# Kernel tuning notes

Measured on AMD Instinct MI355X. Metric: run time of the kernel, lower is better.

## Reference

```python
import jax, jax.numpy as jnp
import numpy as np

D_MODEL = 512
HEADS = 8
WIN = 16
LN_EPS = 1e-5


def setup_inputs() -> dict:
    key = jax.random.key(0)
    ks = jax.random.split(key, 5)
    B, T = 2, 4096
    s = 1.0 / np.sqrt(D_MODEL)
    x = jax.random.normal(ks[0], (B, T, D_MODEL), dtype=jnp.float32)
    Wq = jax.random.normal(ks[1], (D_MODEL, D_MODEL), dtype=jnp.float32) * s
    Wk = jax.random.normal(ks[2], (D_MODEL, D_MODEL), dtype=jnp.float32) * s
    Wv = jax.random.normal(ks[3], (D_MODEL, D_MODEL), dtype=jnp.float32) * s
    Wp = jax.random.normal(ks[4], (D_MODEL, D_MODEL), dtype=jnp.float32) * s
    ln_gamma = jnp.ones((D_MODEL,), dtype=jnp.float32)
    ln_beta = jnp.zeros((D_MODEL,), dtype=jnp.float32)
    return {"x": x, "Wq": Wq, "Wk": Wk, "Wv": Wv, "Wp": Wp,
            "ln_gamma": ln_gamma, "ln_beta": ln_beta}


def _local_attention(x, Wq, Wk, Wv, Wp, ln_gamma, ln_beta):
    B, T, D = x.shape
    H = HEADS
    d = D // H
    scale = d ** (-0.5)
    # projections (torch Linear: y = x @ W^T)
    q = (x @ Wq.T).reshape(B, T, H, d)
    k = (x @ Wk.T).reshape(B, T, H, d)
    v = (x @ Wv.T).reshape(B, T, H, d)
    offs = jnp.arange(-WIN, WIN + 1)                      # [W]
    pos = jnp.arange(T)[:, None] + offs[None, :]          # [T, W]
    valid = (pos >= 0) & (pos < T)                        # [T, W]
    idx = jnp.clip(pos, 0, T - 1)                         # [T, W]
    k_win = k[:, idx]                                     # [B, T, W, H, d]
    v_win = v[:, idx]                                     # [B, T, W, H, d]
    scores = jnp.einsum('bthd,btwhd->bthw', q, k_win) * scale
    scores = jnp.where(valid[None, :, None, :], scores, -jnp.inf)
    attn = jax.nn.softmax(scores, axis=-1)                # over window
    out = jnp.einsum('bthw,btwhd->bthd', attn, v_win).reshape(B, T, D)
    y = x + out @ Wp.T                                    # residual + proj
    mu = jnp.mean(y, axis=-1, keepdims=True)
    var = jnp.mean(jnp.square(y - mu), axis=-1, keepdims=True)
    return ln_gamma * (y - mu) * jax.lax.rsqrt(var + LN_EPS) + ln_beta


def reference(x, Wq, Wk, Wv, Wp, ln_gamma, ln_beta):
    return _local_attention(x, Wq, Wk, Wv, Wp, ln_gamma, ln_beta)
```

## Files before the change

### kernel.cpp

```cpp
#include <hip/hip_runtime.h>
#include <hip/hip_bf16.h>
#include <stdint.h>

typedef __bf16 bf16;
typedef __attribute__((ext_vector_type(8))) __bf16 bf16x8;
typedef __attribute__((ext_vector_type(2))) __bf16 bf16x2;
typedef __attribute__((ext_vector_type(4))) float f32x4;
typedef __attribute__((ext_vector_type(4))) unsigned int u32x4;

#define GLOAD16(gsrc, ldst)                                              \
  __builtin_amdgcn_global_load_lds(                                      \
      (const __attribute__((address_space(1))) unsigned int*)(gsrc),     \
      (__attribute__((address_space(3))) unsigned int*)(ldst), 16, 0, 0)

static constexpr int T_LEN = 4096;
static constexpr int WIN = 16;

__device__ __forceinline__ bf16x8 cvt8(float4 a, float4 b) {
  bf16x8 o;
  o[0] = (bf16)a.x; o[1] = (bf16)a.y; o[2] = (bf16)a.z; o[3] = (bf16)a.w;
  o[4] = (bf16)b.x; o[5] = (bf16)b.y; o[6] = (bf16)b.z; o[7] = (bf16)b.w;
  return o;
}

__global__ __launch_bounds__(256) void prep_kernel(const float* __restrict__ x,
                                                   const float* __restrict__ wq,
                                                   const float* __restrict__ wk,
                                                   const float* __restrict__ wv,
                                                   const float* __restrict__ wp,
                                                   bf16* __restrict__ xb,
                                                   bf16* __restrict__ wqkv,
                                                   bf16* __restrict__ wpb) {
  int bid = blockIdx.x;
  if (bid < 2048) {
    int i = bid * 256 + threadIdx.x;
    const float4* s4 = (const float4*)x + (size_t)i * 2;
    ((bf16x8*)xb)[i] = cvt8(s4[0], s4[1]);
  } else {
    int i = (bid - 2048) * 256 + threadIdx.x;
    int which = i >> 15;
    int j = i & 32767;
    const float* src = (which == 0) ? wq : (which == 1) ? wk : (which == 2) ? wv : wp;
    bf16* dst = (which < 3) ? (wqkv + (size_t)which * 512 * 512) : wpb;
    const float4* s4 = (const float4*)src + (size_t)j * 2;
    ((bf16x8*)dst)[j] = cvt8(s4[0], s4[1]);
  }
}

__global__ __launch_bounds__(256) void gemm_qkv_kernel(const bf16* __restrict__ Ab,
                                                       const bf16* __restrict__ Bw,
                                                       bf16* __restrict__ Cb) {
  constexpr int K = 512, BK = 64, NIT = K / BK;
  __shared__ __align__(16) bf16 SMEM[16384];
  const int tid = threadIdx.x;
  const int l = tid & 63;
  const int w = tid >> 6;
  const int g = l >> 4;
  const int c = l & 15;
  int bid = blockIdx.x;
  bid = (bid & 7) * 96 + (bid >> 3);
  const int m0 = (bid / 12) * 128;
  const int n0 = (bid % 12) * 128;

  const f32x4 zero = {0.f, 0.f, 0.f, 0.f};
  f32x4 acc[4][4];
#pragma unroll
  for (int i = 0; i < 4; ++i)
#pragma unroll
    for (int j = 0; j < 4; ++j) acc[i][j] = zero;

  const int wm = (w >> 1) * 64;
  const int wn = (w & 1) * 64;
  const int cx = c & 7;

#pragma unroll 1
  for (int t = 0; t < NIT; ++t) {
    const int k0 = t * BK;
#pragma unroll
    for (int i = 0; i < 4; ++i) {
      int s = tid + i * 256;
      int row = s >> 3;
      int j = s & 7;
      int ksrc = k0 + ((j ^ (row & 7)) << 3);
      GLOAD16(Ab + (size_t)(m0 + row) * 512 + ksrc, &SMEM[s * 8]);
      GLOAD16(Bw + (size_t)(n0 + row) * 512 + ksrc, &SMEM[8192 + s * 8]);
    }
    __syncthreads();
#pragma unroll
    for (int kk = 0; kk < 2; ++kk) {
      const int joff = ((kk * 4 + g) ^ cx) << 3;
      bf16x8 af[4], bfr[4];
#pragma unroll
      for (int mi = 0; mi < 4; ++mi)
        af[mi] = *(const bf16x8*)&SMEM[(wm + mi * 16 + c) * 64 + joff];
#pragma unroll
      for (int ni = 0; ni < 4; ++ni)
        bfr[ni] = *(const bf16x8*)&SMEM[8192 + (wn + ni * 16 + c) * 64 + joff];
#pragma unroll
      for (int mi = 0; mi < 4; ++mi)
#pragma unroll
        for (int ni = 0; ni < 4; ++ni)
          acc[mi][ni] = __builtin_amdgcn_mfma_f32_16x16x32_bf16(af[mi], bfr[ni], acc[mi][ni], 0, 0, 0);
    }
    __syncthreads();
  }

  bf16* Cw = &SMEM[w * 4096];
  const int r0 = (l >> 4) * 4;
#pragma unroll
  for (int mi = 0; mi < 4; ++mi)
#pragma unroll
    for (int ni = 0; ni < 4; ++ni)
#pragma unroll
      for (int r = 0; r < 4; ++r)
        Cw[(mi * 16 + r0 + r) * 64 + ni * 16 + c] = (bf16)acc[mi][ni][r];
#pragma unroll
  for (int i = 0; i < 8; ++i) {
    int row = (l >> 3) + 8 * i;
    bf16x8 v = *(const bf16x8*)&Cw[row * 64 + (l & 7) * 8];
    *(bf16x8*)(Cb + (size_t)(m0 + wm + row) * 1536 + n0 + wn + (l & 7) * 8) = v;
  }
}

static constexpr int TCB = 64;
static constexpr int NP = 96;
static constexpr int KST = 72;
static constexpr int NPT = 112;

__global__ __launch_bounds__(256) void attn_kernel(const bf16* __restrict__ qkv,
                                                   bf16* __restrict__ aout) {
  __shared__ __align__(16) bf16 Kl[NP * KST];
  __shared__ __align__(16) unsigned short Vt[64 * NPT];
  __shared__ __align__(16) bf16 QPO[4 * 16 * 72];

  const int tid = threadIdx.x;
  const int wid = tid >> 6;
  const int l = tid & 63;
  const int g = l >> 4;
  const int c = l & 15;

  const int bid = blockIdx.x;
  const int chunk = bid & 63;
  const int h = (bid >> 6) & 7;
  const int b = bid >> 9;
  const int t0 = chunk * TCB;
  const int base = b * T_LEN;

#pragma unroll
  for (int i = 0; i < 3; ++i) {
    int task = tid + i * 256;
    int p = task >> 3;
    int c8 = (task & 7) * 8;
    int pg = min(max(t0 - WIN + p, 0), T_LEN - 1);
    const bf16* kr = qkv + (size_t)(base + pg) * 1536 + 512 + h * 64 + c8;
    const bf16* vr = qkv + (size_t)(base + pg) * 1536 + 1024 + h * 64 + c8;
    *(bf16x8*)&Kl[p * KST + c8] = *(const bf16x8*)kr;
    bf16x8 vv = *(const bf16x8*)vr;
#pragma unroll
    for (int e = 0; e < 8; ++e)
      Vt[(c8 + e) * NPT + p] = ((const unsigned short*)&vv)[e];
  }
#pragma unroll
  for (int i = 0; i < 2; ++i) {
    int task = tid + i * 256;
    int p = task >> 3;
    int c8 = (task & 7) * 8;
    const bf16* qr = qkv + (size_t)(base + t0 + p) * 1536 + h * 64 + c8;
    *(bf16x8*)&QPO[(p >> 4) * 1152 + (p & 15) * 72 + c8] = *(const bf16x8*)qr;
  }
  {
    int d = tid >> 2;
    int p0 = 96 + (tid & 3) * 4;
    *(uint2*)&Vt[d * NPT + p0] = make_uint2(0u, 0u);
  }
  __syncthreads();

  const int tg = t0 + wid * 16;
  const float scale = 0.125f;

  bf16* Qw = &QPO[wid * 1152];
  bf16x8 qf0 = *(const bf16x8*)&Qw[c * 72 + g * 8];
  bf16x8 qf1 = *(const bf16x8*)&Qw[c * 72 + 32 + g * 8];

  const f32x4 zero = {0.f, 0.f, 0.f, 0.f};
  const u32x4 zu = {0u, 0u, 0u, 0u};

  f32x4 st[3];
#pragma unroll
  for (int wt = 0; wt < 3; ++wt) {
    int rk = 16 * wid + 16 * wt + c;
    bf16x8 ka0 = *(const bf16x8*)&Kl[rk * KST + g * 8];
    bf16x8 ka1 = *(const bf16x8*)&Kl[rk * KST + 32 + g * 8];
    f32x4 t = __builtin_amdgcn_mfma_f32_16x16x32_bf16(ka0, qf0, zero, 0, 0, 0);
    st[wt] = __builtin_amdgcn_mfma_f32_16x16x32_bf16(ka1, qf1, t, 0, 0, 0);
  }

  float pv[3][4];
  float lsum = 0.f;
#pragma unroll
  for (int wt = 0; wt < 3; ++wt)
#pragma unroll
    for (int r = 0; r < 4; ++r) {
      int w = 16 * wt + 4 * g + r;
      int pos = tg - WIN + w;
      bool valid = (w >= c) && (w <= c + 32) && (pos >= 0) && (pos < T_LEN);
      float e = __expf(st[wt][r] * scale);
      pv[wt][r] = valid ? e : 0.f;
      lsum += pv[wt][r];
    }
  lsum += __shfl_xor(lsum, 16);
  lsum += __shfl_xor(lsum, 32);
  float inv = 1.f / lsum;

  bf16* P = Qw;
#pragma unroll
  for (int wt = 0; wt < 3; ++wt) {
    bf16x2 p01, p23;
    p01[0] = (bf16)(pv[wt][0] * inv);
    p01[1] = (bf16)(pv[wt][1] * inv);
    p23[0] = (bf16)(pv[wt][2] * inv);
    p23[1] = (bf16)(pv[wt][3] * inv);
    *(bf16x2*)&P[c * 56 + 16 * wt + 4 * g]     = p01;
    *(bf16x2*)&P[c * 56 + 16 * wt + 4 * g + 2] = p23;
  }

  bf16x8 pa0 = *(const bf16x8*)&P[c * 56 + 8 * g];
  int g1 = (g < 2) ? g : 1;
  bf16x8 pa1 = *(const bf16x8*)&P[c * 56 + 32 + 8 * g1];
  if (g >= 2) pa1 = __builtin_bit_cast(bf16x8, zu);

  f32x4 acc[4] = {zero, zero, zero, zero};
#pragma unroll
  for (int dt = 0; dt < 4; ++dt) {
    const unsigned short* vp = &Vt[(16 * dt + c) * NPT + 16 * wid + 8 * g];
    bf16x8 v0 = *(const bf16x8*)(vp);
    bf16x8 v1 = *(const bf16x8*)(vp + 32);
    acc[dt] = __builtin_amdgcn_mfma_f32_16x16x32_bf16(pa0, v0, acc[dt], 0, 0, 0);
    acc[dt] = __builtin_amdgcn_mfma_f32_16x16x32_bf16(pa1, v1, acc[dt], 0, 0, 0);
  }

  bf16* O = Qw;
#pragma unroll
  for (int dt = 0; dt < 4; ++dt)
#pragma unroll
    for (int r = 0; r < 4; ++r)
      O[(4 * g + r) * 72 + 16 * dt + c] = (bf16)acc[dt][r];

  bf16x8 o0 = *(const bf16x8*)&O[c * 72 + g * 8];
  bf16x8 o1 = *(const bf16x8*)&O[c * 72 + 32 + g * 8];
  bf16* orow = aout + (size_t)(base + tg + c) * 512 + h * 64;
  *(bf16x8*)(orow + g * 8) = o0;
  *(bf16x8*)(orow + 32 + g * 8) = o1;
}

__global__ __launch_bounds__(512) void proj_ln_kernel(const bf16* __restrict__ A,
                                                      const bf16* __restrict__ Bw,
                                                      const float* __restrict__ X,
                                                      const float* __restrict__ gamma,
                                                      const float* __restrict__ beta,
                                                      float* __restrict__ out) {
  constexpr int K = 512, BK = 64, BM = 32, NIT = K / BK;
  __shared__ __align__(16) bf16 As[BM * BK];
  __shared__ __align__(16) bf16 Bs[512 * BK];
  __shared__ __align__(16) float rsum[32][8];
  __shared__ __align__(16) float rsq[32][8];

  const int tid = threadIdx.x;
  const int w = tid >> 6;
  const int l = tid & 63;
  const int g = l >> 4;
  const int c = l & 15;
  const int cx = c & 7;
  int bid = blockIdx.x;
  bid = (bid & 7) * 32 + (bid >> 3);
  const int m0 = bid * BM;

  const f32x4 zero = {0.f, 0.f, 0.f, 0.f};
  f32x4 acc[2][4];
#pragma unroll
  for (int m = 0; m < 2; ++m)
#pragma unroll
    for (int n = 0; n < 4; ++n) acc[m][n] = zero;

#pragma unroll 1
  for (int t = 0; t < NIT; ++t) {
    const int k0 = t * BK;
    if (tid < 256) {
      int row = tid >> 3;
      int j = tid & 7;
      GLOAD16(A + (size_t)(m0 + row) * 512 + k0 + ((j ^ (row & 7)) << 3), &As[tid * 8]);
    }
#pragma unroll
    for (int i = 0; i < 8; ++i) {
      int s = tid + i * 512;
      int row = s >> 3;
      int j = s & 7;
      GLOAD16(Bw + (size_t)row * 512 + k0 + ((j ^ (row & 7)) << 3), &Bs[s * 8]);
    }
    __syncthreads();
#pragma unroll
    for (int kk = 0; kk < 2; ++kk) {
      const int joff = ((kk * 4 + g) ^ cx) << 3;
      bf16x8 af[2], bfv[4];
#pragma unroll
      for (int m = 0; m < 2; ++m)
        af[m] = *(const bf16x8*)&As[(m * 16 + c) * 64 + joff];
#pragma unroll
      for (int n = 0; n < 4; ++n)
        bfv[n] = *(const bf16x8*)&Bs[(w * 64 + n * 16 + c) * 64 + joff];
#pragma unroll
      for (int m = 0; m < 2; ++m)
#pragma unroll
        for (int n = 0; n < 4; ++n)
          acc[m][n] = __builtin_amdgcn_mfma_f32_16x16x32_bf16(af[m], bfv[n], acc[m][n], 0, 0, 0);
    }
    __syncthreads();
  }

  const int col0 = w * 64 + c;
  float ps[2][4], ps2[2][4];
#pragma unroll
  for (int m = 0; m < 2; ++m)
#pragma unroll
    for (int r = 0; r < 4; ++r) {
      int row = m0 + m * 16 + 4 * g + r;
      float s = 0.f, s2 = 0.f;
#pragma unroll
      for (int n = 0; n < 4; ++n) {
        float y = acc[m][n][r] + X[(size_t)row * 512 + col0 + n * 16];
        acc[m][n][r] = y;
        s += y;
        s2 += y * y;
      }
      ps[m][r] = s;
      ps2[m][r] = s2;
    }
#pragma unroll
  for (int m = 0; m < 2; ++m)
#pragma unroll
    for (int r = 0; r < 4; ++r) {
      float s = ps[m][r], s2 = ps2[m][r];
      s += __shfl_xor(s, 1);  s2 += __shfl_xor(s2, 1);
      s += __shfl_xor(s, 2);  s2 += __shfl_xor(s2, 2);
      s += __shfl_xor(s, 4);  s2 += __shfl_xor(s2, 4);
      s += __shfl_xor(s, 8);  s2 += __shfl_xor(s2, 8);
      ps[m][r] = s;
      ps2[m][r] = s2;
    }
  if (c == 0) {
#pragma unroll
    for (int m = 0; m < 2; ++m)
#pragma unroll
      for (int r = 0; r < 4; ++r) {
        rsum[m * 16 + 4 * g + r][w] = ps[m][r];
        rsq[m * 16 + 4 * g + r][w] = ps2[m][r];
      }
  }
  __syncthreads();

  float gam[4], bet[4];
#pragma unroll
  for (int n = 0; n < 4; ++n) {
    gam[n] = gamma[col0 + n * 16];
    bet[n] = beta[col0 + n * 16];
  }
#pragma unroll
  for (int m = 0; m < 2; ++m)
#pragma unroll
    for (int r = 0; r < 4; ++r) {
      int rl = m * 16 + 4 * g + r;
      float4 s0 = *(const float4*)&rsum[rl][0];
      float4 s1 = *(const float4*)&rsum[rl][4];
      float4 q0 = *(const float4*)&rsq[rl][0];
      float4 q1 = *(const float4*)&rsq[rl][4];
      float sum = (s0.x + s0.y + s0.z + s0.w) + (s1.x + s1.y + s1.z + s1.w);
      float sq  = (q0.x + q0.y + q0.z + q0.w) + (q1.x + q1.y + q1.z + q1.w);
      float mu = sum * (1.f / 512.f);
      float var = sq * (1.f / 512.f) - mu * mu;
      float rs = rsqrtf(var + 1e-5f);
#pragma unroll
      for (int n = 0; n < 4; ++n)
        out[(size_t)(m0 + rl) * 512 + col0 + n * 16] =
            gam[n] * (acc[m][n][r] - mu) * rs + bet[n];
    }
}

extern "C" void kernel_launch(void* const* d_in, const int* in_sizes, int n_in,
                              void* d_out, int out_size, void* d_ws, size_t ws_size,
                              hipStream_t stream) {
  const float* x  = (const float*)d_in[0];
  const float* Wq = (const float*)d_in[1];
  const float* Wk = (const float*)d_in[2];
  const float* Wv = (const float*)d_in[3];
  const float* Wp = (const float*)d_in[4];
  const float* g  = (const float*)d_in[5];
  const float* be = (const float*)d_in[6];
  float* out = (float*)d_out;

  char* ws = (char*)d_ws;
  bf16* xb   = (bf16*)(ws);
  bf16* wqkv = (bf16*)(ws + 8388608);
  bf16* wpb  = (bf16*)(ws + 9961472);
  bf16* qkv  = (bf16*)(ws + 10485760);
  bf16* aout = (bf16*)(ws + 35651584);

  prep_kernel<<<2560, 256, 0, stream>>>(x, Wq, Wk, Wv, Wp, xb, wqkv, wpb);
  gemm_qkv_kernel<<<64 * 12, 256, 0, stream>>>(xb, wqkv, qkv);
  attn_kernel<<<1024, 256, 0, stream>>>(qkv, aout);
  proj_ln_kernel<<<256, 512, 0, stream>>>(aout, wpb, x, g, be, out);
}
```

Measured before the change: 60.81 us.

## Fuse sliding-window attention into projection+LayerNorm kernel, keep attention output in LDS

Merges the attention kernel into the output-projection/LayerNorm kernel. Each 512-thread block computes attention for its 32 rows across all 8 heads in two passes of 4 heads, writes the result into an LDS tile, then runs the Wp GEMM directly from that tile. This removes one kernel launch and the global write and read of the intermediate attention output. In exchange, only 256 blocks do the attention work (previously 1024), LDS use per block is large (~127KB), and the K/V windows are loaded per 32-row block with more halo overlap.

Result: faster. 59.58 us (-2.0%).

```diff
diff --git a/kernel.cpp b/kernel.cpp
--- a/kernel.cpp
+++ b/kernel.cpp
@@ -62,16 +62,16 @@
   const int m0 = (bid / 12) * 128;
   const int n0 = (bid % 12) * 128;
 
-  const f32x4 zero = {0.f, 0.f, 0.f, 0.f};
-  f32x4 acc[4][4];
-#pragma unroll
-  for (int i = 0; i < 4; ++i)
-#pragma unroll
-    for (int j = 0; j < 4; ++j) acc[i][j] = zero;
-
   const int wm = (w >> 1) * 64;
   const int wn = (w & 1) * 64;
   const int cx = c & 7;
+
+  const f32x4 zero = {0.f, 0.f, 0.f, 0.f};
+  f32x4 acc[4][4];
+#pragma unroll
+  for (int i = 0; i < 4; ++i)
+#pragma unroll
+    for (int j = 0; j < 4; ++j) acc[i][j] = zero;
 
 #pragma unroll 1
   for (int t = 0; t < NIT; ++t) {
@@ -122,148 +122,16 @@
   }
 }
 
-static constexpr int TCB = 64;
-static constexpr int NP = 96;
-static constexpr int KST = 72;
-static constexpr int NPT = 112;
-
-__global__ __launch_bounds__(256) void attn_kernel(const bf16* __restrict__ qkv,
-                                                   bf16* __restrict__ aout) {
-  __shared__ __align__(16) bf16 Kl[NP * KST];
-  __shared__ __align__(16) unsigned short Vt[64 * NPT];
-  __shared__ __align__(16) bf16 QPO[4 * 16 * 72];
-
-  const int tid = threadIdx.x;
-  const int wid = tid >> 6;
-  const int l = tid & 63;
-  const int g = l >> 4;
-  const int c = l & 15;
-
-  const int bid = blockIdx.x;
-  const int chunk = bid & 63;
-  const int h = (bid >> 6) & 7;
-  const int b = bid >> 9;
-  const int t0 = chunk * TCB;
-  const int base = b * T_LEN;
-
-#pragma unroll
-  for (int i = 0; i < 3; ++i) {
-    int task = tid + i * 256;
-    int p = task >> 3;
-    int c8 = (task & 7) * 8;
-    int pg = min(max(t0 - WIN + p, 0), T_LEN - 1);
-    const bf16* kr = qkv + (size_t)(base + pg) * 1536 + 512 + h * 64 + c8;
-    const bf16* vr = qkv + (size_t)(base + pg) * 1536 + 1024 + h * 64 + c8;
-    *(bf16x8*)&Kl[p * KST + c8] = *(const bf16x8*)kr;
-    bf16x8 vv = *(const bf16x8*)vr;
-#pragma unroll
-    for (int e = 0; e < 8; ++e)
-      Vt[(c8 + e) * NPT + p] = ((const unsigned short*)&vv)[e];
-  }
-#pragma unroll
-  for (int i = 0; i < 2; ++i) {
-    int task = tid + i * 256;
-    int p = task >> 3;
-    int c8 = (task & 7) * 8;
-    const bf16* qr = qkv + (size_t)(base + t0 + p) * 1536 + h * 64 + c8;
-    *(bf16x8*)&QPO[(p >> 4) * 1152 + (p & 15) * 72 + c8] = *(const bf16x8*)qr;
-  }
-  {
-    int d = tid >> 2;
-    int p0 = 96 + (tid & 3) * 4;
-    *(uint2*)&Vt[d * NPT + p0] = make_uint2(0u, 0u);
-  }
-  __syncthreads();
-
-  const int tg = t0 + wid * 16;
-  const float scale = 0.125f;
-
-  bf16* Qw = &QPO[wid * 1152];
-  bf16x8 qf0 = *(const bf16x8*)&Qw[c * 72 + g * 8];
-  bf16x8 qf1 = *(const bf16x8*)&Qw[c * 72 + 32 + g * 8];
-
-  const f32x4 zero = {0.f, 0.f, 0.f, 0.f};
-  const u32x4 zu = {0u, 0u, 0u, 0u};
-
-  f32x4 st[3];
-#pragma unroll
-  for (int wt = 0; wt < 3; ++wt) {
-    int rk = 16 * wid + 16 * wt + c;
-    bf16x8 ka0 = *(const bf16x8*)&Kl[rk * KST + g * 8];
-    bf16x8 ka1 = *(const bf16x8*)&Kl[rk * KST + 32 + g * 8];
-    f32x4 t = __builtin_amdgcn_mfma_f32_16x16x32_bf16(ka0, qf0, zero, 0, 0, 0);
-    st[wt] = __builtin_amdgcn_mfma_f32_16x16x32_bf16(ka1, qf1, t, 0, 0, 0);
-  }
-
-  float pv[3][4];
-  float lsum = 0.f;
-#pragma unroll
-  for (int wt = 0; wt < 3; ++wt)
-#pragma unroll
-    for (int r = 0; r < 4; ++r) {
-      int w = 16 * wt + 4 * g + r;
-      int pos = tg - WIN + w;
-      bool valid = (w >= c) && (w <= c + 32) && (pos >= 0) && (pos < T_LEN);
-      float e = __expf(st[wt][r] * scale);
-      pv[wt][r] = valid ? e : 0.f;
-      lsum += pv[wt][r];
-    }
-  lsum += __shfl_xor(lsum, 16);
-  lsum += __shfl_xor(lsum, 32);
-  float inv = 1.f / lsum;
-
-  bf16* P = Qw;
-#pragma unroll
-  for (int wt = 0; wt < 3; ++wt) {
-    bf16x2 p01, p23;
-    p01[0] = (bf16)(pv[wt][0] * inv);
-    p01[1] = (bf16)(pv[wt][1] * inv);
-    p23[0] = (bf16)(pv[wt][2] * inv);
-    p23[1] = (bf16)(pv[wt][3] * inv);
-    *(bf16x2*)&P[c * 56 + 16 * wt + 4 * g]     = p01;
-    *(bf16x2*)&P[c * 56 + 16 * wt + 4 * g + 2] = p23;
-  }
-
-  bf16x8 pa0 = *(const bf16x8*)&P[c * 56 + 8 * g];
-  int g1 = (g < 2) ? g : 1;
-  bf16x8 pa1 = *(const bf16x8*)&P[c * 56 + 32 + 8 * g1];
-  if (g >= 2) pa1 = __builtin_bit_cast(bf16x8, zu);
-
-  f32x4 acc[4] = {zero, zero, zero, zero};
-#pragma unroll
-  for (int dt = 0; dt < 4; ++dt) {
-    const unsigned short* vp = &Vt[(16 * dt + c) * NPT + 16 * wid + 8 * g];
-    bf16x8 v0 = *(const bf16x8*)(vp);
-    bf16x8 v1 = *(const bf16x8*)(vp + 32);
-    acc[dt] = __builtin_amdgcn_mfma_f32_16x16x32_bf16(pa0, v0, acc[dt], 0, 0, 0);
-    acc[dt] = __builtin_amdgcn_mfma_f32_16x16x32_bf16(pa1, v1, acc[dt], 0, 0, 0);
-  }
-
-  bf16* O = Qw;
-#pragma unroll
-  for (int dt = 0; dt < 4; ++dt)
-#pragma unroll
-    for (int r = 0; r < 4; ++r)
-      O[(4 * g + r) * 72 + 16 * dt + c] = (bf16)acc[dt][r];
-
-  bf16x8 o0 = *(const bf16x8*)&O[c * 72 + g * 8];
-  bf16x8 o1 = *(const bf16x8*)&O[c * 72 + 32 + g * 8];
-  bf16* orow = aout + (size_t)(base + tg + c) * 512 + h * 64;
-  *(bf16x8*)(orow + g * 8) = o0;
-  *(bf16x8*)(orow + 32 + g * 8) = o1;
-}
-
-__global__ __launch_bounds__(512) void proj_ln_kernel(const bf16* __restrict__ A,
-                                                      const bf16* __restrict__ Bw,
-                                                      const float* __restrict__ X,
-                                                      const float* __restrict__ gamma,
-                                                      const float* __restrict__ beta,
-                                                      float* __restrict__ out) {
-  constexpr int K = 512, BK = 64, BM = 32, NIT = K / BK;
-  __shared__ __align__(16) bf16 As[BM * BK];
-  __shared__ __align__(16) bf16 Bs[512 * BK];
-  __shared__ __align__(16) float rsum[32][8];
-  __shared__ __align__(16) float rsq[32][8];
+__global__ __launch_bounds__(512) void attn_proj_ln_kernel(
+    const bf16* __restrict__ qkv, const bf16* __restrict__ Bw,
+    const float* __restrict__ X, const float* __restrict__ gamma,
+    const float* __restrict__ beta, float* __restrict__ out) {
+  __shared__ __align__(16) bf16 POOL[63744];
+  bf16* KV = POOL;
+  bf16* Pp = POOL + 36864;
+  bf16* aoutL = POOL + 46080;
+  float* rsum = (float*)(POOL + 62720);
+  float* rsq  = (float*)(POOL + 63232);
 
   const int tid = threadIdx.x;
   const int w = tid >> 6;
@@ -273,29 +141,126 @@
   const int cx = c & 7;
   int bid = blockIdx.x;
   bid = (bid & 7) * 32 + (bid >> 3);
-  const int m0 = bid * BM;
+  const int m0 = bid * 32;
+  const int b = m0 >> 12;
+  const int tloc0 = m0 & (T_LEN - 1);
+  const int base = b * T_LEN;
 
   const f32x4 zero = {0.f, 0.f, 0.f, 0.f};
-  f32x4 acc[2][4];
+  const u32x4 zu = {0u, 0u, 0u, 0u};
+  const float scale = 0.125f;
+
+#pragma unroll 1
+  for (int pass = 0; pass < 2; ++pass) {
+    if (pass) __syncthreads();
+#pragma unroll
+    for (int i = 0; i < 4; ++i) {
+      int task = tid + i * 512;
+      int hl = task >> 9;
+      int rem = task & 511;
+      int pp = rem >> 3;
+      int c8 = (rem & 7) * 8;
+      int h = pass * 4 + hl;
+      int pg = base + min(max(tloc0 - WIN + pp, 0), T_LEN - 1);
+      const bf16* kr = qkv + (size_t)pg * 1536 + 512 + h * 64 + c8;
+      const bf16* vr = qkv + (size_t)pg * 1536 + 1024 + h * 64 + c8;
+      *(bf16x8*)&KV[hl * 4608 + pp * 72 + c8] = *(const bf16x8*)kr;
+      bf16x8 vv = *(const bf16x8*)vr;
+      bf16* vt = &KV[18432 + hl * 4608];
+#pragma unroll
+      for (int e = 0; e < 8; ++e) vt[(c8 + e) * 72 + pp] = vv[e];
+    }
+    __syncthreads();
+
+    const int hl = w >> 1;
+    const int wh = w & 1;
+    const int h = pass * 4 + hl;
+    const int tg = tloc0 + wh * 16;
+    bf16* Kl = &KV[hl * 4608];
+    bf16* Vt = &KV[18432 + hl * 4608];
+
+    const bf16* qrow = qkv + (size_t)(base + tg + c) * 1536 + h * 64;
+    bf16x8 qf0 = *(const bf16x8*)(qrow + g * 8);
+    bf16x8 qf1 = *(const bf16x8*)(qrow + 32 + g * 8);
+
+    f32x4 st[3];
+#pragma unroll
+    for (int wt = 0; wt < 3; ++wt) {
+      int rk = 16 * wh + 16 * wt + c;
+      bf16x8 ka0 = *(const bf16x8*)&Kl[rk * 72 + g * 8];
+      bf16x8 ka1 = *(const bf16x8*)&Kl[rk * 72 + 32 + g * 8];
+      f32x4 t = __builtin_amdgcn_mfma_f32_16x16x32_bf16(ka0, qf0, zero, 0, 0, 0);
+      st[wt] = __builtin_amdgcn_mfma_f32_16x16x32_bf16(ka1, qf1, t, 0, 0, 0);
+    }
+
+    float pv[3][4];
+    float lsum = 0.f;
+#pragma unroll
+    for (int wt = 0; wt < 3; ++wt)
+#pragma unroll
+      for (int r = 0; r < 4; ++r) {
+        int ww = 16 * wt + 4 * g + r;
+        int pos = tg - WIN + ww;
+        bool valid = (ww >= c) && (ww <= c + 32) && (pos >= 0) && (pos < T_LEN);
+        float e = __expf(st[wt][r] * scale);
+        pv[wt][r] = valid ? e : 0.f;
+        lsum += pv[wt][r];
+      }
+    lsum += __shfl_xor(lsum, 16);
+    lsum += __shfl_xor(lsum, 32);
+    float inv = 1.f / lsum;
+
+    bf16* P = &Pp[w * 1152];
+#pragma unroll
+    for (int wt = 0; wt < 3; ++wt) {
+      bf16x2 p01, p23;
+      p01[0] = (bf16)(pv[wt][0] * inv);
+      p01[1] = (bf16)(pv[wt][1] * inv);
+      p23[0] = (bf16)(pv[wt][2] * inv);
+      p23[1] = (bf16)(pv[wt][3] * inv);
+      *(bf16x2*)&P[c * 56 + 16 * wt + 4 * g]     = p01;
+      *(bf16x2*)&P[c * 56 + 16 * wt + 4 * g + 2] = p23;
+    }
+
+    bf16x8 pa0 = *(const bf16x8*)&P[c * 56 + 8 * g];
+    int g1 = (g < 2) ? g : 1;
+    bf16x8 pa1 = *(const bf16x8*)&P[c * 56 + 32 + 8 * g1];
+    if (g >= 2) pa1 = __builtin_bit_cast(bf16x8, zu);
+
+    const int off0 = 16 * wh + 8 * g;
+    const int off1 = 16 * wh + ((g < 2) ? 32 + 8 * g : 48);
+    f32x4 acc[4] = {zero, zero, zero, zero};
+#pragma unroll
+    for (int dt = 0; dt < 4; ++dt) {
+      bf16x8 v0 = *(const bf16x8*)&Vt[(16 * dt + c) * 72 + off0];
+      bf16x8 v1 = *(const bf16x8*)&Vt[(16 * dt + c) * 72 + off1];
+      acc[dt] = __builtin_amdgcn_mfma_f32_16x16x32_bf16(pa0, v0, acc[dt], 0, 0, 0);
+      acc[dt] = __builtin_amdgcn_mfma_f32_16x16x32_bf16(pa1, v1, acc[dt], 0, 0, 0);
+    }
+
+#pragma unroll
+    for (int dt = 0; dt < 4; ++dt)
+#pragma unroll
+      for (int r = 0; r < 4; ++r)
+        aoutL[(wh * 16 + 4 * g + r) * 520 + h * 64 + 16 * dt + c] = (bf16)acc[dt][r];
+  }
+  __syncthreads();
+
+  f32x4 acc2[2][4];
 #pragma unroll
   for (int m = 0; m < 2; ++m)
 #pragma unroll
-    for (int n = 0; n < 4; ++n) acc[m][n] = zero;
+    for (int n = 0; n < 4; ++n) acc2[m][n] = zero;
 
 #pragma unroll 1
-  for (int t = 0; t < NIT; ++t) {
-    const int k0 = t * BK;
-    if (tid < 256) {
-      int row = tid >> 3;
-      int j = tid & 7;
-      GLOAD16(A + (size_t)(m0 + row) * 512 + k0 + ((j ^ (row & 7)) << 3), &As[tid * 8]);
-    }
+  for (int t = 0; t < 8; ++t) {
+    const int k0 = t * 64;
 #pragma unroll
     for (int i = 0; i < 8; ++i) {
       int s = tid + i * 512;
       int row = s >> 3;
       int j = s & 7;
-      GLOAD16(Bw + (size_t)row * 512 + k0 + ((j ^ (row & 7)) << 3), &Bs[s * 8]);
+      GLOAD16(Bw + (size_t)row * 512 + k0 + ((j ^ (row & 7)) << 3), &KV[s * 8]);
     }
     __syncthreads();
 #pragma unroll
@@ -304,15 +269,15 @@
       bf16x8 af[2], bfv[4];
 #pragma unroll
       for (int m = 0; m < 2; ++m)
-        af[m] = *(const bf16x8*)&As[(m * 16 + c) * 64 + joff];
+        af[m] = *(const bf16x8*)&aoutL[(m * 16 + c) * 520 + k0 + (kk * 4 + g) * 8];
 #pragma unroll
       for (int n = 0; n < 4; ++n)
-        bfv[n] = *(const bf16x8*)&Bs[(w * 64 + n * 16 + c) * 64 + joff];
+        bfv[n] = *(const bf16x8*)&KV[(w * 64 + n * 16 + c) * 64 + joff];
 #pragma unroll
       for (int m = 0; m < 2; ++m)
 #pragma unroll
         for (int n = 0; n < 4; ++n)
-          acc[m][n] = __builtin_amdgcn_mfma_f32_16x16x32_bf16(af[m], bfv[n], acc[m][n], 0, 0, 0);
+          acc2[m][n] = __builtin_amdgcn_mfma_f32_16x16x32_bf16(af[m], bfv[n], acc2[m][n], 0, 0, 0);
     }
     __syncthreads();
   }
@@ -327,8 +292,8 @@
       float s = 0.f, s2 = 0.f;
 #pragma unroll
       for (int n = 0; n < 4; ++n) {
-        float y = acc[m][n][r] + X[(size_t)row * 512 + col0 + n * 16];
-        acc[m][n][r] = y;
+        float y = acc2[m][n][r] + X[(size_t)row * 512 + col0 + n * 16];
+        acc2[m][n][r] = y;
         s += y;
         s2 += y * y;
       }
@@ -352,8 +317,8 @@
     for (int m = 0; m < 2; ++m)
 #pragma unroll
       for (int r = 0; r < 4; ++r) {
-        rsum[m * 16 + 4 * g + r][w] = ps[m][r];
-        rsq[m * 16 + 4 * g + r][w] = ps2[m][r];
+        rsum[(m * 16 + 4 * g + r) * 8 + w] = ps[m][r];
+        rsq[(m * 16 + 4 * g + r) * 8 + w] = ps2[m][r];
       }
   }
   __syncthreads();
@@ -369,19 +334,19 @@
 #pragma unroll
     for (int r = 0; r < 4; ++r) {
       int rl = m * 16 + 4 * g + r;
-      float4 s0 = *(const float4*)&rsum[rl][0];
-      float4 s1 = *(const float4*)&rsum[rl][4];
-      float4 q0 = *(const float4*)&rsq[rl][0];
-      float4 q1 = *(const float4*)&rsq[rl][4];
-      float sum = (s0.x + s0.y + s0.z + s0.w) + (s1.x + s1.y + s1.z + s1.w);
-      float sq  = (q0.x + q0.y + q0.z + q0.w) + (q1.x + q1.y + q1.z + q1.w);
+      float sum = 0.f, sq = 0.f;
+#pragma unroll
+      for (int j = 0; j < 8; ++j) {
+        sum += rsum[rl * 8 + j];
+        sq += rsq[rl * 8 + j];
+      }
       float mu = sum * (1.f / 512.f);
       float var = sq * (1.f / 512.f) - mu * mu;
       float rs = rsqrtf(var + 1e-5f);
 #pragma unroll
       for (int n = 0; n < 4; ++n)
         out[(size_t)(m0 + rl) * 512 + col0 + n * 16] =
-            gam[n] * (acc[m][n][r] - mu) * rs + bet[n];
+            gam[n] * (acc2[m][n][r] - mu) * rs + bet[n];
     }
 }
 
@@ -402,10 +367,8 @@
   bf16* wqkv = (bf16*)(ws + 8388608);
   bf16* wpb  = (bf16*)(ws + 9961472);
   bf16* qkv  = (bf16*)(ws + 10485760);
-  bf16* aout = (bf16*)(ws + 35651584);
 
   prep_kernel<<<2560, 256, 0, stream>>>(x, Wq, Wk, Wv, Wp, xb, wqkv, wpb);
   gemm_qkv_kernel<<<64 * 12, 256, 0, stream>>>(xb, wqkv, qkv);
-  attn_kernel<<<1024, 256, 0, stream>>>(qkv, aout);
-  proj_ln_kernel<<<256, 512, 0, stream>>>(aout, wpb, x, g, be, out);
-}
+  attn_proj_ln_kernel<<<256, 512, 0, stream>>>(qkv, wpb, x, g, be, out);
+}
```
